# Kernel tuning notes

Hardware: AMD Instinct MI355X
Metric: run time of the kernel (lower is better)

The kernel has to match this reference:

```python
import jax, jax.numpy as jnp
import numpy as np

TEMP = 0.5  # init kwarg `tmp`
NUM_CLASSES = 100


def setup_inputs() -> dict:
    key = jax.random.key(0)
    k1, k2 = jax.random.split(key)
    embedding = jax.random.normal(k1, (8192, 256), dtype=jnp.float32)
    label = jax.random.randint(k2, (8192,), 0, NUM_CLASSES, dtype=jnp.int64)
    return {"embedding": embedding, "label": label}


def reference(embedding, label):
    # Row-normalize -> pairwise cosine similarity [N, N]
    normed = embedding / jnp.linalg.norm(embedding, axis=1, keepdims=True)
    sim = (normed @ normed.T) / TEMP  # already divided by temperature

    N = embedding.shape[0]
    eye = jnp.eye(N, dtype=bool)

    # Denominator: sum of exp(sim) over off-diagonal entries per row
    exp_sim = jnp.exp(sim)
    row_sum = jnp.sum(jnp.where(eye, 0.0, exp_sim), axis=1)  # [N]

    # log(exp(sim_ij) / row_sum_i) = sim_ij - log(row_sum_i)
    log_prob = sim - jnp.log(row_sum)[:, None]

    # Positive mask: same label, i != j
    pos_mask = (label[:, None] == label[None, :]) & ~eye
    n_i = jnp.sum(pos_mask, axis=1)  # positives per anchor

    inner = jnp.sum(jnp.where(pos_mask, log_prob, 0.0), axis=1)  # [N]
    per_anchor = jnp.where(n_i > 0, -inner / jnp.maximum(n_i, 1).astype(sim.dtype), 0.0)
    return jnp.sum(per_anchor)
```

## Files before the change

kernel.cpp:

```cpp
#include <hip/hip_runtime.h>
#include <hip/hip_bf16.h>
#include <stdint.h>

#define N    8192
#define D    256
#define NCLS 100

static constexpr float TEMP    = 0.5f;
static constexpr float SCALE_F = 1.69864360f;
static constexpr float LN2     = 0.69314718055994531f;

#define NSLOT 130

typedef float f32x4 __attribute__((ext_vector_type(4)));
typedef long  lx2  __attribute__((ext_vector_type(2)));

__device__ __forceinline__ unsigned short f2bf(float f) {
  union { float f; unsigned int u; } x; x.f = f;
  unsigned int r = x.u + 0x7fffu + ((x.u >> 16) & 1u);
  return (unsigned short)(r >> 16);
}
__device__ __forceinline__ float bf2f(unsigned short b) {
  union { unsigned int u; float f; } x; x.u = ((unsigned int)b) << 16;
  return x.f;
}


__global__ __launch_bounds__(256) void normalize_kernel(
    const float* __restrict__ emb, const long long* __restrict__ label,
    unsigned short* __restrict__ abf, unsigned char* __restrict__ a8,
    int* __restrict__ cnt, int* __restrict__ list) {
  const int row  = blockIdx.x * 4 + (threadIdx.x >> 6);
  const int lane = threadIdx.x & 63;
  const float4 v = ((const float4*)(emb + (size_t)row * D))[lane];
  float ss = v.x * v.x + v.y * v.y + v.z * v.z + v.w * v.w;
#pragma unroll
  for (int off = 1; off < 64; off <<= 1) ss += __shfl_xor(ss, off);
  const float s = rsqrtf(ss) * SCALE_F;
  const float x = v.x * s, y = v.y * s, z = v.z * s, wv = v.w * s;

  ushort4 o;
  o.x = f2bf(x); o.y = f2bf(y); o.z = f2bf(z); o.w = f2bf(wv);
  ((ushort4*)(abf + (size_t)row * D))[lane] = o;

  int p = __builtin_amdgcn_cvt_pk_fp8_f32(x, y, 0, false);
  p = __builtin_amdgcn_cvt_pk_fp8_f32(z, wv, p, true);
  *(int*)(a8 + (size_t)(row >> 4) * 4096 + (lane >> 4) * 1024 +
          ((lane >> 1) & 3) * 256 + (row & 15) * 16 + ((lane >> 3) & 1) * 8 +
          (lane & 1) * 4) = p;

  if (lane == 0) {
    const int c = (int)label[row];
    const int slot = atomicAdd(cnt + c, 1);
    list[c * 256 + slot] = row;
  }
}

struct TileCoord { int x, y; };
__device__ __forceinline__ TileCoord tri_decode(int b) {
  int x = (int)((-1.0f + sqrtf(1.0f + 8.0f * (float)b)) * 0.5f);
  while ((x + 1) * (x + 2) / 2 <= b) ++x;
  while (x * (x + 1) / 2 > b) --x;
  return {x, b - x * (x + 1) / 2};
}

__global__ __launch_bounds__(256, 2) void simexp_rowsum_kernel(
    const unsigned char* __restrict__ A, float* __restrict__ part) {
  const int tid  = threadIdx.x;
  const int w    = tid >> 6;
  const int lane = tid & 63;
  const int quad = lane >> 4;
  const int l15  = lane & 15;

  const TileCoord tc = tri_decode(blockIdx.x);
  const int x = tc.x, y = tc.y;
  const int row0 = y << 7;
  const int col0 = x << 7;
  const bool diag = (x == y);
  const int wm  = (w & 1) * 64;
  const int jn0 = (w >> 1) * 64;

  if (diag && wm > jn0) {
    part[((size_t)y * NSLOT + 2 * x) * 128 + 64 + lane] = 0.f;
    part[((size_t)x * NSLOT + 129) * 128 + lane] = 0.f;
    return;
  }
  const bool needmask = diag && (wm == jn0);

  const unsigned char* Ap = A + (size_t)((row0 >> 4) + (w & 1) * 4) * 4096;
  const unsigned char* Bp = A + (size_t)((col0 >> 4) + (w >> 1) * 4) * 4096;
  const int lo = quad * 256 + l15 * 16;

  lx2 aF[4][4], bF[4][4];
#pragma unroll
  for (int mt = 0; mt < 4; ++mt)
#pragma unroll
    for (int kq = 0; kq < 4; ++kq)
      aF[mt][kq] = *(const lx2*)(Ap + mt * 4096 + kq * 1024 + lo);
#pragma unroll
  for (int nt = 0; nt < 4; ++nt)
#pragma unroll
    for (int kq = 0; kq < 4; ++kq)
      bF[nt][kq] = *(const lx2*)(Bp + nt * 4096 + kq * 1024 + lo);

  f32x4 acc[4][4];
#pragma unroll
  for (int mt = 0; mt < 4; ++mt)
#pragma unroll
    for (int nt = 0; nt < 4; ++nt) acc[mt][nt] = (f32x4){0.f, 0.f, 0.f, 0.f};

#pragma unroll
  for (int kq = 0; kq < 4; ++kq)
#pragma unroll
    for (int kkl = 0; kkl < 2; ++kkl)
#pragma unroll
      for (int mt = 0; mt < 4; ++mt)
#pragma unroll
        for (int nt = 0; nt < 4; ++nt)
          acc[mt][nt] = __builtin_amdgcn_mfma_f32_16x16x32_fp8_fp8(
              aF[mt][kq][kkl], bF[nt][kq][kkl], acc[mt][nt], 0, 0, 0);

  float rowpart[4][4];
  float colpart[4] = {0.f, 0.f, 0.f, 0.f};
#pragma unroll
  for (int mt = 0; mt < 4; ++mt)
#pragma unroll
    for (int e = 0; e < 4; ++e) rowpart[mt][e] = 0.f;
#pragma unroll
  for (int mt = 0; mt < 4; ++mt)
#pragma unroll
    for (int nt = 0; nt < 4; ++nt)
#pragma unroll
      for (int e = 0; e < 4; ++e) {
        float v = __builtin_amdgcn_exp2f(acc[mt][nt][e]);
        if (needmask) {
          const int iw = mt * 16 + quad * 4 + e;
          const int jw = nt * 16 + l15;
          v = (iw < jw) ? v : 0.f;
        }
        rowpart[mt][e] += v;
        colpart[nt] += v;
      }

  const int rslot = 2 * x + (jn0 >> 6);
  const int cslot = diag ? (128 + (wm >> 6)) : (2 * y + (wm >> 6));
  float* rowdst = part + ((size_t)y * NSLOT + rslot) * 128 + wm;
  float* coldst = part + ((size_t)x * NSLOT + cslot) * 128 + jn0;

#pragma unroll
  for (int nt = 0; nt < 4; ++nt) {
    float v = colpart[nt];
    v += __shfl_xor(v, 16);
    v += __shfl_xor(v, 32);
    if (quad == 0) coldst[nt * 16 + l15] = v;
  }
#pragma unroll
  for (int mt = 0; mt < 4; ++mt)
#pragma unroll
    for (int e = 0; e < 4; ++e) {
      float v = rowpart[mt][e];
      v += __shfl_xor(v, 1);
      v += __shfl_xor(v, 2);
      v += __shfl_xor(v, 4);
      v += __shfl_xor(v, 8);
      if (l15 == 0) rowdst[mt * 16 + quad * 4 + e] = v;
    }
}

__global__ __launch_bounds__(256) void finalize_kernel(
    const unsigned short* __restrict__ abf, const float* __restrict__ part,
    const long long* __restrict__ label, const int* __restrict__ cnt,
    const int* __restrict__ list, float* __restrict__ out) {
  __shared__ float red[4];
  __shared__ int rows_l[256];
  const int tid  = threadIdx.x;
  const int w    = tid >> 6;
  const int lane = tid & 63;

  if (blockIdx.x < NCLS) {
    const int c = blockIdx.x;
    const int m = cnt[c];
    if (m <= 1) return;
    if (tid < m) rows_l[tid] = list[c * 256 + tid];
    __syncthreads();
    float acc = 0.f;
    for (int s = 0; s < m; ++s)
      acc += bf2f(abf[(size_t)rows_l[s] * D + tid]);
    float v = acc * acc;
#pragma unroll
    for (int off = 1; off < 64; off <<= 1) v += __shfl_xor(v, off);
    if (lane == 0) red[w] = v;
    __syncthreads();
    if (tid == 0) {
      const float ssq = red[0] + red[1] + red[2] + red[3];
      const float term = (ssq * LN2 - 2.0f * (float)m) / (float)(m - 1);
      atomicAdd(out, -term);
    }
  } else {
    const int i = (blockIdx.x - NCLS) * 256 + tid;
    const int band = i >> 7, r = i & 127;
    const float* ps = part + (size_t)band * NSLOT * 128 + r;
    float rs = 0.f;
#pragma unroll 13
    for (int s = 0; s < NSLOT; ++s) rs += ps[(size_t)s * 128];
    const int c = (int)label[i];
    float v = 0.f;
    if (cnt[c] > 1)
      v = __builtin_amdgcn_logf(rs) * LN2;
#pragma unroll
    for (int off = 1; off < 64; off <<= 1) v += __shfl_xor(v, off);
    if (lane == 0) red[w] = v;
    __syncthreads();
    if (tid == 0)
      atomicAdd(out, red[0] + red[1] + red[2] + red[3]);
  }
}

extern "C" void kernel_launch(void* const* d_in, const int* in_sizes, int n_in,
                              void* d_out, int out_size, void* d_ws,
                              size_t ws_size, hipStream_t stream) {
  const float* emb = (const float*)d_in[0];
  const long long* label = (const long long*)d_in[1];
  float* out = (float*)d_out;

  char* ws = (char*)d_ws;
  unsigned short* abf = (unsigned short*)ws;
  unsigned char* a8 = (unsigned char*)(ws + (size_t)N * D * 2);
  float* part = (float*)(ws + (size_t)N * D * 3);
  int* cnt = (int*)(ws + (size_t)N * D * 3 + (size_t)64 * NSLOT * 128 * 4);
  int* list = cnt + 128;

  hipMemsetAsync(cnt, 0, 128 * 4, stream);
  hipMemsetAsync(out, 0, sizeof(float), stream);

  normalize_kernel<<<N / 4, 256, 0, stream>>>(emb, label, abf, a8, cnt, list);

  simexp_rowsum_kernel<<<2080, 256, 0, stream>>>(a8, part);

  finalize_kernel<<<NCLS + N / 256, 256, 0, stream>>>(abf, part, label, cnt,
                                                      list, out);
}
```

Before: 122.6 us.

## Process two column tiles per block reusing A fragments in similarity kernel

```diff
diff --git a/kernel.cpp b/kernel.cpp
--- a/kernel.cpp
+++ b/kernel.cpp
@@ -10,7 +10,7 @@
 static constexpr float SCALE_F = 1.69864360f;
 static constexpr float LN2     = 0.69314718055994531f;
 
-#define NSLOT 130
+#define NSLOT 192
 
 typedef float f32x4 __attribute__((ext_vector_type(4)));
 typedef long  lx2  __attribute__((ext_vector_type(2)));
@@ -56,14 +56,6 @@
   }
 }
 
-struct TileCoord { int x, y; };
-__device__ __forceinline__ TileCoord tri_decode(int b) {
-  int x = (int)((-1.0f + sqrtf(1.0f + 8.0f * (float)b)) * 0.5f);
-  while ((x + 1) * (x + 2) / 2 <= b) ++x;
-  while (x * (x + 1) / 2 > b) --x;
-  return {x, b - x * (x + 1) / 2};
-}
-
 __global__ __launch_bounds__(256, 2) void simexp_rowsum_kernel(
     const unsigned char* __restrict__ A, float* __restrict__ part) {
   const int tid  = threadIdx.x;
@@ -72,88 +64,93 @@
   const int quad = lane >> 4;
   const int l15  = lane & 15;
 
-  const TileCoord tc = tri_decode(blockIdx.x);
-  const int x = tc.x, y = tc.y;
-  const int row0 = y << 7;
-  const int col0 = x << 7;
-  const bool diag = (x == y);
+  const int b = blockIdx.x;
+  int y = 0, c = 0;
+  while (c + ((65 - y) >> 1) <= b) { c += (65 - y) >> 1; ++y; }
+  const int s = b - c;
+
   const int wm  = (w & 1) * 64;
   const int jn0 = (w >> 1) * 64;
-
-  if (diag && wm > jn0) {
-    part[((size_t)y * NSLOT + 2 * x) * 128 + 64 + lane] = 0.f;
-    part[((size_t)x * NSLOT + 129) * 128 + lane] = 0.f;
-    return;
-  }
-  const bool needmask = diag && (wm == jn0);
-
-  const unsigned char* Ap = A + (size_t)((row0 >> 4) + (w & 1) * 4) * 4096;
-  const unsigned char* Bp = A + (size_t)((col0 >> 4) + (w >> 1) * 4) * 4096;
+  const int jh  = jn0 >> 6;
+  const int wh  = wm >> 6;
+  const bool diagstrip = (s == 0);
+
+  const unsigned char* Ap = A + (size_t)(y * 8 + (w & 1) * 4) * 4096;
   const int lo = quad * 256 + l15 * 16;
 
-  lx2 aF[4][4], bF[4][4];
+  lx2 aF[4][4];
 #pragma unroll
   for (int mt = 0; mt < 4; ++mt)
 #pragma unroll
     for (int kq = 0; kq < 4; ++kq)
       aF[mt][kq] = *(const lx2*)(Ap + mt * 4096 + kq * 1024 + lo);
-#pragma unroll
-  for (int nt = 0; nt < 4; ++nt)
+
+  float rowpart[4][4];
+#pragma unroll
+  for (int mt = 0; mt < 4; ++mt)
+#pragma unroll
+    for (int e = 0; e < 4; ++e) rowpart[mt][e] = 0.f;
+
+#pragma unroll
+  for (int t = 0; t < 2; ++t) {
+    const int x = y + 2 * s + t;
+    if (x >= 64) break;
+
+    const unsigned char* Bp = A + (size_t)(x * 8 + (w >> 1) * 4) * 4096;
+    lx2 bF[4][4];
+#pragma unroll
+    for (int nt = 0; nt < 4; ++nt)
+#pragma unroll
+      for (int kq = 0; kq < 4; ++kq)
+        bF[nt][kq] = *(const lx2*)(Bp + nt * 4096 + kq * 1024 + lo);
+
+    f32x4 acc[4][4];
+#pragma unroll
+    for (int mt = 0; mt < 4; ++mt)
+#pragma unroll
+      for (int nt = 0; nt < 4; ++nt)
+        acc[mt][nt] = (f32x4){0.f, 0.f, 0.f, 0.f};
+
 #pragma unroll
     for (int kq = 0; kq < 4; ++kq)
-      bF[nt][kq] = *(const lx2*)(Bp + nt * 4096 + kq * 1024 + lo);
-
-  f32x4 acc[4][4];
-#pragma unroll
-  for (int mt = 0; mt < 4; ++mt)
-#pragma unroll
-    for (int nt = 0; nt < 4; ++nt) acc[mt][nt] = (f32x4){0.f, 0.f, 0.f, 0.f};
-
-#pragma unroll
-  for (int kq = 0; kq < 4; ++kq)
-#pragma unroll
-    for (int kkl = 0; kkl < 2; ++kkl)
-#pragma unroll
-      for (int mt = 0; mt < 4; ++mt)
-#pragma unroll
-        for (int nt = 0; nt < 4; ++nt)
-          acc[mt][nt] = __builtin_amdgcn_mfma_f32_16x16x32_fp8_fp8(
-              aF[mt][kq][kkl], bF[nt][kq][kkl], acc[mt][nt], 0, 0, 0);
-
-  float rowpart[4][4];
-  float colpart[4] = {0.f, 0.f, 0.f, 0.f};
-#pragma unroll
-  for (int mt = 0; mt < 4; ++mt)
-#pragma unroll
-    for (int e = 0; e < 4; ++e) rowpart[mt][e] = 0.f;
-#pragma unroll
-  for (int mt = 0; mt < 4; ++mt)
-#pragma unroll
-    for (int nt = 0; nt < 4; ++nt)
-#pragma unroll
-      for (int e = 0; e < 4; ++e) {
-        float v = __builtin_amdgcn_exp2f(acc[mt][nt][e]);
-        if (needmask) {
-          const int iw = mt * 16 + quad * 4 + e;
-          const int jw = nt * 16 + l15;
-          v = (iw < jw) ? v : 0.f;
+#pragma unroll
+      for (int kkl = 0; kkl < 2; ++kkl)
+#pragma unroll
+        for (int mt = 0; mt < 4; ++mt)
+#pragma unroll
+          for (int nt = 0; nt < 4; ++nt)
+            acc[mt][nt] = __builtin_amdgcn_mfma_f32_16x16x32_fp8_fp8(
+                aF[mt][kq][kkl], bF[nt][kq][kkl], acc[mt][nt], 0, 0, 0);
+
+    const bool dmask = diagstrip && (t == 0);
+    float colpart[4] = {0.f, 0.f, 0.f, 0.f};
+#pragma unroll
+    for (int mt = 0; mt < 4; ++mt)
+#pragma unroll
+      for (int nt = 0; nt < 4; ++nt)
+#pragma unroll
+        for (int e = 0; e < 4; ++e) {
+          float v = __builtin_amdgcn_exp2f(acc[mt][nt][e]);
+          if (dmask) {
+            const int iw = wm + mt * 16 + quad * 4 + e;
+            const int jw = jn0 + nt * 16 + l15;
+            v = (iw < jw) ? v : 0.f;
+          }
+          rowpart[mt][e] += v;
+          colpart[nt] += v;
         }
-        rowpart[mt][e] += v;
-        colpart[nt] += v;
-      }
-
-  const int rslot = 2 * x + (jn0 >> 6);
-  const int cslot = diag ? (128 + (wm >> 6)) : (2 * y + (wm >> 6));
-  float* rowdst = part + ((size_t)y * NSLOT + rslot) * 128 + wm;
-  float* coldst = part + ((size_t)x * NSLOT + cslot) * 128 + jn0;
-
-#pragma unroll
-  for (int nt = 0; nt < 4; ++nt) {
-    float v = colpart[nt];
-    v += __shfl_xor(v, 16);
-    v += __shfl_xor(v, 32);
-    if (quad == 0) coldst[nt * 16 + l15] = v;
+
+    float* coldst = part + ((size_t)x * NSLOT + 64 + 2 * y + wh) * 128 + jn0;
+#pragma unroll
+    for (int nt = 0; nt < 4; ++nt) {
+      float v = colpart[nt];
+      v += __shfl_xor(v, 16);
+      v += __shfl_xor(v, 32);
+      if (quad == 0) coldst[nt * 16 + l15] = v;
+    }
   }
+
+  float* rowdst = part + ((size_t)y * NSLOT + 2 * s + jh) * 128 + wm;
 #pragma unroll
   for (int mt = 0; mt < 4; ++mt)
 #pragma unroll
@@ -200,9 +197,11 @@
     const int i = (blockIdx.x - NCLS) * 256 + tid;
     const int band = i >> 7, r = i & 127;
     const float* ps = part + (size_t)band * NSLOT * 128 + r;
+    const int rs_n = 2 * ((65 - band) >> 1);
+    const int cs_n = 2 * band + 2;
     float rs = 0.f;
-#pragma unroll 13
-    for (int s = 0; s < NSLOT; ++s) rs += ps[(size_t)s * 128];
+    for (int s2 = 0; s2 < rs_n; ++s2) rs += ps[(size_t)s2 * 128];
+    for (int u = 0; u < cs_n; ++u) rs += ps[(size_t)(64 + u) * 128];
     const int c = (int)label[i];
     float v = 0.f;
     if (cnt[c] > 1)
@@ -235,7 +234,7 @@
 
   normalize_kernel<<<N / 4, 256, 0, stream>>>(emb, label, abf, a8, cnt, list);
 
-  simexp_rowsum_kernel<<<2080, 256, 0, stream>>>(a8, part);
+  simexp_rowsum_kernel<<<1056, 256, 0, stream>>>(a8, part);
 
   finalize_kernel<<<NCLS + N / 256, 256, 0, stream>>>(abf, part, label, cnt,
                                                       list, out);
```

After: 149.5 us. 21.9% more time.
